# Optimization experiments

Hardware: AMD Instinct MI355X
Metric: run time of the kernel (lower is better)

Reference implementation:

```python
import jax, jax.numpy as jnp
import numpy as np

B, N, D = 64, 2048, 128  # batch, neighbors, embedding_dim (= region_dim)


def setup_inputs() -> dict:
    key = jax.random.key(0)
    ks = jax.random.split(key, 8)
    inv_sqrt_d = 1.0 / np.sqrt(D).astype(np.float32)
    return {
        "e_i": jax.random.normal(ks[0], (B, D), jnp.float32),
        "e_j": jax.random.normal(ks[1], (B, N, D), jnp.float32),
        "imp_j": jax.random.uniform(ks[2], (B, N), jnp.float32),
        "R_lk": jax.random.normal(ks[3], (D, D), jnp.float32),
        "W_q": jax.random.normal(ks[4], (D, D), jnp.float32) * inv_sqrt_d,
        "W_k": jax.random.normal(ks[5], (D, D), jnp.float32) * inv_sqrt_d,
        "W_v": jax.random.normal(ks[6], (D, D), jnp.float32) * inv_sqrt_d,
        "omega": jax.random.normal(ks[7], (D,), jnp.float32),
    }


def reference(e_i, e_j, imp_j, R_lk, W_q, W_k, W_v, omega):
    # torch nn.Linear(x) = x @ W.T; weights are [out, in] = [D, D]
    q = e_i @ W_q.T                                   # [B, D]
    k = jnp.einsum('bnd,ed->bne', e_j, W_k)           # [B, N, D]
    # additive tanh attention score sigma_ij = tanh(q_i + k_j) . omega
    sigma = jnp.tanh(q[:, None, :] + k) @ omega       # [B, N]
    exp_s = jnp.exp(sigma)
    denom = jnp.sum(exp_s, axis=1, keepdims=True) + 1e-9
    a = imp_j * exp_s / denom                         # [B, N]  (a_ij, squeezed)
    v = jnp.einsum('bnd,ed->bne', e_j, W_v)           # [B, N, D]
    # A_i_t = sum_n a_ij * v_j  (identical math to A_i_l in the source)
    A_l = jnp.einsum('bn,bnd->bd', a, v)              # [B, D]
    # sum_n R[l,k] * a[b,n] * v[b,n,k] = R[l,k] * A_l[b,k]  -- fused, no [B,N,D,D]
    A_lk = R_lk[None, :, :] * A_l[:, None, :]         # [B, D, D]
    return A_l, A_lk, A_l
```

## Files before the change

kernel.cpp:

```cpp
#include <hip/hip_runtime.h>
#include <stdint.h>

#define BB 64
#define NN 2048
#define DD 128
#define ROWS 64
#define CPB 2

typedef __attribute__((ext_vector_type(8))) short short8;
typedef __attribute__((ext_vector_type(4))) float f32x4;

__device__ __forceinline__ unsigned short f2bf_rtne(float x) {
    union { float f; unsigned int u; } v; v.f = x;
    unsigned int r = v.u + 0x7fffu + ((v.u >> 16) & 1u);
    return (unsigned short)(r >> 16);
}
__device__ __forceinline__ float bf2f(unsigned short h) {
    union { unsigned int u; float f; } v; v.u = ((unsigned int)h) << 16;
    return v.f;
}
__device__ __forceinline__ float tanh_fast(float x) {
    float ax = fabsf(x);
    float e  = __expf(-2.f * ax);
    float t  = (1.f - e) / (1.f + e);
    return copysignf(t, x);
}
__device__ __forceinline__ void ldsbar() {
    asm volatile("s_waitcnt lgkmcnt(0)" ::: "memory");
    __builtin_amdgcn_s_barrier();
}

__global__ __launch_bounds__(256) void aegis_prep(
    const float* __restrict__ e_i, const float* __restrict__ Wq,
    const float* __restrict__ Wk,
    float* __restrict__ qbuf, unsigned short* __restrict__ Bhig,
    unsigned short* __restrict__ Blog,
    float* __restrict__ sprime, float* __restrict__ denom)
{
    __shared__ float eis[DD];
    const int t = threadIdx.x, blk = blockIdx.x;
    if (blk < 8) {
        const int tid = blk * 256 + t;
        const int lr = tid & 15, lg = (tid >> 4) & 3, ks = (tid >> 6) & 3, et = tid >> 8;
        const int e = et * 16 + lr, k = ks * 32 + lg * 8;
        const float* src = Wk + e * DD + k;
        float4 x0 = *reinterpret_cast<const float4*>(src);
        float4 x1 = *reinterpret_cast<const float4*>(src + 4);
        float xs[8] = {x0.x, x0.y, x0.z, x0.w, x1.x, x1.y, x1.z, x1.w};
        short8 h, l;
        #pragma unroll
        for (int j = 0; j < 8; ++j) {
            unsigned short hb = f2bf_rtne(xs[j]);
            float rem = xs[j] - bf2f(hb);
            h[j] = (short)hb;
            l[j] = (short)f2bf_rtne(rem);
        }
        *reinterpret_cast<short8*>(Bhig + (size_t)tid * 8) = h;
        *reinterpret_cast<short8*>(Blog + (size_t)tid * 8) = l;
    } else {
        const int b = blk - 8;
        if (t < DD) eis[t] = e_i[b * DD + t];
        __syncthreads();
        if (t < DD) {
            float acc = 0.f;
            const float4* wr = reinterpret_cast<const float4*>(Wq + t * DD);
            const float4* ev = reinterpret_cast<const float4*>(eis);
            #pragma unroll 8
            for (int i = 0; i < 32; ++i) {
                float4 w = wr[i], e = ev[i];
                acc = fmaf(w.x, e.x, acc); acc = fmaf(w.y, e.y, acc);
                acc = fmaf(w.z, e.z, acc); acc = fmaf(w.w, e.w, acc);
            }
            qbuf[b * DD + t] = acc;
            sprime[b * DD + t] = 0.f;
        }
        if (t == 0) denom[b] = 0.f;
    }
}

__global__ __launch_bounds__(256, 3) void aegis_main(
    const float* __restrict__ e_j, const float* __restrict__ imp,
    const float* __restrict__ omega, const float* __restrict__ qbuf,
    const unsigned short* __restrict__ Bhig, const unsigned short* __restrict__ Blog,
    float* __restrict__ sprime, float* __restrict__ denom)
{
    __shared__ unsigned short Ehi[ROWS * DD];
    __shared__ unsigned short Elo[ROWS * DD];
    __shared__ float sig[ROWS][4];
    __shared__ float wrow[ROWS];
    __shared__ float scolq[4][DD];

    const int t    = threadIdx.x;
    const int b    = blockIdx.x >> 4;
    const int cb   = blockIdx.x & 15;
    const int lane = t & 63;
    const int w    = t >> 6;
    const int lr   = lane & 15;
    const int lg   = lane >> 4;
    const int row0 = cb * (CPB * ROWS);

    float4 st[8];
    const float4* ejp = reinterpret_cast<const float4*>(
        e_j + (size_t)(b * NN + row0) * DD);
    #pragma unroll
    for (int i = 0; i < 8; ++i) st[i] = ejp[t + i * 256];

    short8 Bh[2][4], Bl[2][4];
    #pragma unroll
    for (int ct = 0; ct < 2; ++ct)
        #pragma unroll
        for (int ks = 0; ks < 4; ++ks) {
            const int fi = (((2 * w + ct) * 4 + ks) * 4 + lg) * 16 + lr;
            Bh[ct][ks] = *reinterpret_cast<const short8*>(Bhig + (size_t)fi * 8);
            Bl[ct][ks] = *reinterpret_cast<const short8*>(Blog + (size_t)fi * 8);
        }

    float qv[2], ov[2];
    #pragma unroll
    for (int ct = 0; ct < 2; ++ct) {
        const int c = 32 * w + 16 * ct + lr;
        qv[ct] = qbuf[b * DD + c];
        ov[ct] = omega[c];
    }
    float impv[CPB];
    if (t < ROWS) {
        #pragma unroll
        for (int c = 0; c < CPB; ++c) impv[c] = imp[b * NN + row0 + c * ROWS + t];
    }

    #pragma unroll
    for (int i = 0; i < 8; ++i) {
        const int idx = t + i * 256;
        const int rr  = idx >> 5;
        const int bc  = (idx & 31) * 8;
        float xs[4] = {st[i].x, st[i].y, st[i].z, st[i].w};
        unsigned short hs[4], ls[4];
        #pragma unroll
        for (int j = 0; j < 4; ++j) {
            hs[j] = f2bf_rtne(xs[j]);
            ls[j] = f2bf_rtne(xs[j] - bf2f(hs[j]));
        }
        uint2 ph, pl;
        ph.x = (unsigned)hs[0] | ((unsigned)hs[1] << 16);
        ph.y = (unsigned)hs[2] | ((unsigned)hs[3] << 16);
        pl.x = (unsigned)ls[0] | ((unsigned)ls[1] << 16);
        pl.y = (unsigned)ls[2] | ((unsigned)ls[3] << 16);
        const int off = rr * 256 + (bc ^ ((rr & 7) << 4));
        *reinterpret_cast<uint2*>(reinterpret_cast<char*>(Ehi) + off) = ph;
        *reinterpret_cast<uint2*>(reinterpret_cast<char*>(Elo) + off) = pl;
    }
    #pragma unroll
    for (int i = 0; i < 8; ++i) st[i] = ejp[2048 + t + i * 256];

    ldsbar();

    float sacc = 0.f, den_local = 0.f;
    const int rq = t >> 6;
    const int cp = t & 63;

    #pragma unroll
    for (int c = 0; c < CPB; ++c) {
        #pragma unroll 1
        for (int rt = 0; rt < 4; ++rt) {
            f32x4 a0 = {0.f, 0.f, 0.f, 0.f};
            f32x4 a1 = {0.f, 0.f, 0.f, 0.f};
            const int arow  = rt * 16 + lr;
            const int rbase = arow * 256;
            const int rsw   = (lr & 7) << 4;
            #pragma unroll
            for (int ks = 0; ks < 4; ++ks) {
                const int off = rbase + ((ks * 64 + lg * 16) ^ rsw);
                short8 ah = *reinterpret_cast<const short8*>(
                    reinterpret_cast<const char*>(Ehi) + off);
                short8 al = *reinterpret_cast<const short8*>(
                    reinterpret_cast<const char*>(Elo) + off);
                a0 = __builtin_amdgcn_mfma_f32_16x16x32_bf16(ah, Bh[0][ks], a0, 0, 0, 0);
                a1 = __builtin_amdgcn_mfma_f32_16x16x32_bf16(ah, Bh[1][ks], a1, 0, 0, 0);
                a0 = __builtin_amdgcn_mfma_f32_16x16x32_bf16(ah, Bl[0][ks], a0, 0, 0, 0);
                a1 = __builtin_amdgcn_mfma_f32_16x16x32_bf16(ah, Bl[1][ks], a1, 0, 0, 0);
                a0 = __builtin_amdgcn_mfma_f32_16x16x32_bf16(al, Bh[0][ks], a0, 0, 0, 0);
                a1 = __builtin_amdgcn_mfma_f32_16x16x32_bf16(al, Bh[1][ks], a1, 0, 0, 0);
            }
            float sp[4];
            #pragma unroll
            for (int i = 0; i < 4; ++i) {
                float x0 = qv[0] + a0[i];
                float x1 = qv[1] + a1[i];
                sp[i] = fmaf(ov[0], tanh_fast(x0), ov[1] * tanh_fast(x1));
            }
            #pragma unroll
            for (int m = 1; m < 16; m <<= 1) {
                #pragma unroll
                for (int i = 0; i < 4; ++i) sp[i] += __shfl_xor(sp[i], m);
            }
            if (lr == 0) {
                #pragma unroll
                for (int i = 0; i < 4; ++i) sig[rt * 16 + 4 * lg + i][w] = sp[i];
            }
        }
        ldsbar();

        if (t < ROWS) {
            float sg = sig[t][0] + sig[t][1] + sig[t][2] + sig[t][3];
            float es = __expf(sg);
            wrow[t]  = es * impv[c];
            float ds = es;
            #pragma unroll
            for (int m = 1; m < 64; m <<= 1) ds += __shfl_xor(ds, m);
            if (t == 0) den_local += ds;
        }
        ldsbar();

        {
            float a0 = 0.f, a1 = 0.f;
            #pragma unroll
            for (int j = 0; j < 16; ++j) {
                const int rr  = rq * 16 + j;
                const int off = rr * 256 + ((4 * cp) ^ ((rr & 7) << 4));
                const unsigned hbits = *reinterpret_cast<const unsigned*>(
                    reinterpret_cast<const char*>(Ehi) + off);
                const unsigned lbits = *reinterpret_cast<const unsigned*>(
                    reinterpret_cast<const char*>(Elo) + off);
                const float wv = wrow[rr];
                float v0 = bf2f((unsigned short)hbits) + bf2f((unsigned short)lbits);
                float v1 = bf2f((unsigned short)(hbits >> 16)) + bf2f((unsigned short)(lbits >> 16));
                a0 = fmaf(wv, v0, a0);
                a1 = fmaf(wv, v1, a1);
            }
            scolq[rq][2 * cp]     = a0;
            scolq[rq][2 * cp + 1] = a1;
        }
        ldsbar();

        if (t < DD) sacc += scolq[0][t] + scolq[1][t] + scolq[2][t] + scolq[3][t];

        if (c + 1 < CPB) {
            #pragma unroll
            for (int i = 0; i < 8; ++i) {
                const int idx = t + i * 256;
                const int rr  = idx >> 5;
                const int bc  = (idx & 31) * 8;
                float xs[4] = {st[i].x, st[i].y, st[i].z, st[i].w};
                unsigned short hs[4], ls[4];
                #pragma unroll
                for (int j = 0; j < 4; ++j) {
                    hs[j] = f2bf_rtne(xs[j]);
                    ls[j] = f2bf_rtne(xs[j] - bf2f(hs[j]));
                }
                uint2 ph, pl;
                ph.x = (unsigned)hs[0] | ((unsigned)hs[1] << 16);
                ph.y = (unsigned)hs[2] | ((unsigned)hs[3] << 16);
                pl.x = (unsigned)ls[0] | ((unsigned)ls[1] << 16);
                pl.y = (unsigned)ls[2] | ((unsigned)ls[3] << 16);
                const int off = rr * 256 + (bc ^ ((rr & 7) << 4));
                *reinterpret_cast<uint2*>(reinterpret_cast<char*>(Ehi) + off) = ph;
                *reinterpret_cast<uint2*>(reinterpret_cast<char*>(Elo) + off) = pl;
            }
            ldsbar();
        }
    }

    if (t < DD) atomicAdd(&sprime[b * DD + t], sacc);
    if (t == 0) atomicAdd(&denom[b], den_local);
}

__global__ __launch_bounds__(256) void aegis_epi(
    const float* __restrict__ sprime, const float* __restrict__ denomv,
    const float* __restrict__ Wv, const float* __restrict__ R,
    float* __restrict__ out)
{
    __shared__ float sn[DD];
    __shared__ float alred[DD][2];
    __shared__ float al[DD];
    const int t = threadIdx.x, b = blockIdx.x;

    if (t < DD) sn[t] = sprime[b * DD + t] / (denomv[b] + 1e-9f);
    __syncthreads();
    {
        const int l = t >> 1, h = t & 1;
        const float4* wr = reinterpret_cast<const float4*>(Wv + l * DD + h * 64);
        const float4* sv = reinterpret_cast<const float4*>(sn + h * 64);
        float acc = 0.f;
        #pragma unroll 8
        for (int i = 0; i < 16; ++i) {
            float4 w = wr[i], e = sv[i];
            acc = fmaf(w.x, e.x, acc); acc = fmaf(w.y, e.y, acc);
            acc = fmaf(w.z, e.z, acc); acc = fmaf(w.w, e.w, acc);
        }
        alred[l][h] = acc;
    }
    __syncthreads();
    if (t < DD) {
        float v = alred[t][0] + alred[t][1];
        al[t] = v;
        out[b * DD + t] = v;
        out[8192 + 1048576 + b * DD + t] = v;
    }
    __syncthreads();
    float4* dst = reinterpret_cast<float4*>(out + 8192 + (size_t)b * DD * DD);
    const float4* rsrc = reinterpret_cast<const float4*>(R);
    #pragma unroll
    for (int i = 0; i < 16; ++i) {
        const int idx = t + i * 256;
        float4 r = rsrc[idx];
        const int k0 = (idx & 31) * 4;
        float4 o;
        o.x = r.x * al[k0];     o.y = r.y * al[k0 + 1];
        o.z = r.z * al[k0 + 2]; o.w = r.w * al[k0 + 3];
        dst[idx] = o;
    }
}

extern "C" void kernel_launch(void* const* d_in, const int* in_sizes, int n_in,
                              void* d_out, int out_size, void* d_ws, size_t ws_size,
                              hipStream_t stream) {
    const float* e_i = (const float*)d_in[0];
    const float* e_j = (const float*)d_in[1];
    const float* imp = (const float*)d_in[2];
    const float* R   = (const float*)d_in[3];
    const float* Wq  = (const float*)d_in[4];
    const float* Wk  = (const float*)d_in[5];
    const float* Wv  = (const float*)d_in[6];
    const float* om  = (const float*)d_in[7];

    float* out    = (float*)d_out;
    float* sprime = (float*)d_ws;
    float* denom  = (float*)((char*)d_ws + 32768);

    float* qbuf = out + 8192;
    unsigned short* Bhig = (unsigned short*)(out + 8192 + 8192);
    unsigned short* Blog = Bhig + 16384;

    aegis_prep<<<dim3(72), dim3(256), 0, stream>>>(
        e_i, Wq, Wk, qbuf, Bhig, Blog, sprime, denom);
    aegis_main<<<dim3(BB * 16), dim3(256), 0, stream>>>(
        e_j, imp, om, qbuf, Bhig, Blog, sprime, denom);
    aegis_epi<<<dim3(BB), dim3(256), 0, stream>>>(sprime, denom, Wv, R, out);
}
```

Baseline: 153.3 us.

## Process one 64-row chunk per block and double the main-kernel grid

The main kernel now gives each block a single 64-row chunk instead of two, and launches twice as many blocks (BB*32). This removes the in-block register prefetch of the second chunk and the per-chunk loop, so each block needs fewer registers, and the launch bound no longer requests three blocks per CU. The cost is twice as many atomicAdds into sprime and denom, plus the setup repeated in every block (loading the B fragments, q and omega). The block also loses its overlap of the next chunk's global load with the current chunk's compute.

Measured after the change: 133.9 us. 1.15x faster.

```diff
diff --git a/kernel.cpp b/kernel.cpp
--- a/kernel.cpp
+++ b/kernel.cpp
@@ -5,7 +5,6 @@
 #define NN 2048
 #define DD 128
 #define ROWS 64
-#define CPB 2
 
 typedef __attribute__((ext_vector_type(8))) short short8;
 typedef __attribute__((ext_vector_type(4))) float f32x4;
@@ -78,7 +77,7 @@
     }
 }
 
-__global__ __launch_bounds__(256, 3) void aegis_main(
+__global__ __launch_bounds__(256) void aegis_main(
     const float* __restrict__ e_j, const float* __restrict__ imp,
     const float* __restrict__ omega, const float* __restrict__ qbuf,
     const unsigned short* __restrict__ Bhig, const unsigned short* __restrict__ Blog,
@@ -90,14 +89,14 @@
     __shared__ float wrow[ROWS];
     __shared__ float scolq[4][DD];
 
-    const int t    = threadIdx.x;
-    const int b    = blockIdx.x >> 4;
-    const int cb   = blockIdx.x & 15;
-    const int lane = t & 63;
-    const int w    = t >> 6;
-    const int lr   = lane & 15;
-    const int lg   = lane >> 4;
-    const int row0 = cb * (CPB * ROWS);
+    const int t     = threadIdx.x;
+    const int b     = blockIdx.x >> 5;
+    const int chunk = blockIdx.x & 31;
+    const int row0  = chunk * ROWS;
+    const int lane  = t & 63;
+    const int w     = t >> 6;
+    const int lr    = lane & 15;
+    const int lg    = lane >> 4;
 
     float4 st[8];
     const float4* ejp = reinterpret_cast<const float4*>(
@@ -122,11 +121,7 @@
         qv[ct] = qbuf[b * DD + c];
         ov[ct] = omega[c];
     }
-    float impv[CPB];
-    if (t < ROWS) {
-        #pragma unroll
-        for (int c = 0; c < CPB; ++c) impv[c] = imp[b * NN + row0 + c * ROWS + t];
-    }
+    const float impv = (t < ROWS) ? imp[b * NN + row0 + t] : 0.f;
 
     #pragma unroll
     for (int i = 0; i < 8; ++i) {
@@ -149,118 +144,86 @@
         *reinterpret_cast<uint2*>(reinterpret_cast<char*>(Ehi) + off) = ph;
         *reinterpret_cast<uint2*>(reinterpret_cast<char*>(Elo) + off) = pl;
     }
-    #pragma unroll
-    for (int i = 0; i < 8; ++i) st[i] = ejp[2048 + t + i * 256];
-
     ldsbar();
 
-    float sacc = 0.f, den_local = 0.f;
-    const int rq = t >> 6;
-    const int cp = t & 63;
-
-    #pragma unroll
-    for (int c = 0; c < CPB; ++c) {
-        #pragma unroll 1
-        for (int rt = 0; rt < 4; ++rt) {
-            f32x4 a0 = {0.f, 0.f, 0.f, 0.f};
-            f32x4 a1 = {0.f, 0.f, 0.f, 0.f};
-            const int arow  = rt * 16 + lr;
-            const int rbase = arow * 256;
-            const int rsw   = (lr & 7) << 4;
+    #pragma unroll 1
+    for (int rt = 0; rt < 4; ++rt) {
+        f32x4 a0 = {0.f, 0.f, 0.f, 0.f};
+        f32x4 a1 = {0.f, 0.f, 0.f, 0.f};
+        const int rbase = (rt * 16 + lr) * 256;
+        const int rsw   = (lr & 7) << 4;
+        #pragma unroll
+        for (int ks = 0; ks < 4; ++ks) {
+            const int off = rbase + ((ks * 64 + lg * 16) ^ rsw);
+            short8 ah = *reinterpret_cast<const short8*>(
+                reinterpret_cast<const char*>(Ehi) + off);
+            short8 al = *reinterpret_cast<const short8*>(
+                reinterpret_cast<const char*>(Elo) + off);
+            a0 = __builtin_amdgcn_mfma_f32_16x16x32_bf16(ah, Bh[0][ks], a0, 0, 0, 0);
+            a1 = __builtin_amdgcn_mfma_f32_16x16x32_bf16(ah, Bh[1][ks], a1, 0, 0, 0);
+            a0 = __builtin_amdgcn_mfma_f32_16x16x32_bf16(ah, Bl[0][ks], a0, 0, 0, 0);
+            a1 = __builtin_amdgcn_mfma_f32_16x16x32_bf16(ah, Bl[1][ks], a1, 0, 0, 0);
+            a0 = __builtin_amdgcn_mfma_f32_16x16x32_bf16(al, Bh[0][ks], a0, 0, 0, 0);
+            a1 = __builtin_amdgcn_mfma_f32_16x16x32_bf16(al, Bh[1][ks], a1, 0, 0, 0);
+        }
+        float sp[4];
+        #pragma unroll
+        for (int i = 0; i < 4; ++i) {
+            float x0 = qv[0] + a0[i];
+            float x1 = qv[1] + a1[i];
+            sp[i] = fmaf(ov[0], tanh_fast(x0), ov[1] * tanh_fast(x1));
+        }
+        #pragma unroll
+        for (int m = 1; m < 16; m <<= 1) {
             #pragma unroll
-            for (int ks = 0; ks < 4; ++ks) {
-                const int off = rbase + ((ks * 64 + lg * 16) ^ rsw);
-                short8 ah = *reinterpret_cast<const short8*>(
-                    reinterpret_cast<const char*>(Ehi) + off);
-                short8 al = *reinterpret_cast<const short8*>(
-                    reinterpret_cast<const char*>(Elo) + off);
-                a0 = __builtin_amdgcn_mfma_f32_16x16x32_bf16(ah, Bh[0][ks], a0, 0, 0, 0);
-                a1 = __builtin_amdgcn_mfma_f32_16x16x32_bf16(ah, Bh[1][ks], a1, 0, 0, 0);
-                a0 = __builtin_amdgcn_mfma_f32_16x16x32_bf16(ah, Bl[0][ks], a0, 0, 0, 0);
-                a1 = __builtin_amdgcn_mfma_f32_16x16x32_bf16(ah, Bl[1][ks], a1, 0, 0, 0);
-                a0 = __builtin_amdgcn_mfma_f32_16x16x32_bf16(al, Bh[0][ks], a0, 0, 0, 0);
-                a1 = __builtin_amdgcn_mfma_f32_16x16x32_bf16(al, Bh[1][ks], a1, 0, 0, 0);
-            }
-            float sp[4];
+            for (int i = 0; i < 4; ++i) sp[i] += __shfl_xor(sp[i], m);
+        }
+        if (lr == 0) {
             #pragma unroll
-            for (int i = 0; i < 4; ++i) {
-                float x0 = qv[0] + a0[i];
-                float x1 = qv[1] + a1[i];
-                sp[i] = fmaf(ov[0], tanh_fast(x0), ov[1] * tanh_fast(x1));
-            }
-            #pragma unroll
-            for (int m = 1; m < 16; m <<= 1) {
-                #pragma unroll
-                for (int i = 0; i < 4; ++i) sp[i] += __shfl_xor(sp[i], m);
-            }
-            if (lr == 0) {
-                #pragma unroll
-                for (int i = 0; i < 4; ++i) sig[rt * 16 + 4 * lg + i][w] = sp[i];
-            }
-        }
-        ldsbar();
-
-        if (t < ROWS) {
-            float sg = sig[t][0] + sig[t][1] + sig[t][2] + sig[t][3];
-            float es = __expf(sg);
-            wrow[t]  = es * impv[c];
-            float ds = es;
-            #pragma unroll
-            for (int m = 1; m < 64; m <<= 1) ds += __shfl_xor(ds, m);
-            if (t == 0) den_local += ds;
-        }
-        ldsbar();
-
-        {
-            float a0 = 0.f, a1 = 0.f;
-            #pragma unroll
-            for (int j = 0; j < 16; ++j) {
-                const int rr  = rq * 16 + j;
-                const int off = rr * 256 + ((4 * cp) ^ ((rr & 7) << 4));
-                const unsigned hbits = *reinterpret_cast<const unsigned*>(
-                    reinterpret_cast<const char*>(Ehi) + off);
-                const unsigned lbits = *reinterpret_cast<const unsigned*>(
-                    reinterpret_cast<const char*>(Elo) + off);
-                const float wv = wrow[rr];
-                float v0 = bf2f((unsigned short)hbits) + bf2f((unsigned short)lbits);
-                float v1 = bf2f((unsigned short)(hbits >> 16)) + bf2f((unsigned short)(lbits >> 16));
-                a0 = fmaf(wv, v0, a0);
-                a1 = fmaf(wv, v1, a1);
-            }
-            scolq[rq][2 * cp]     = a0;
-            scolq[rq][2 * cp + 1] = a1;
-        }
-        ldsbar();
-
-        if (t < DD) sacc += scolq[0][t] + scolq[1][t] + scolq[2][t] + scolq[3][t];
-
-        if (c + 1 < CPB) {
-            #pragma unroll
-            for (int i = 0; i < 8; ++i) {
-                const int idx = t + i * 256;
-                const int rr  = idx >> 5;
-                const int bc  = (idx & 31) * 8;
-                float xs[4] = {st[i].x, st[i].y, st[i].z, st[i].w};
-                unsigned short hs[4], ls[4];
-                #pragma unroll
-                for (int j = 0; j < 4; ++j) {
-                    hs[j] = f2bf_rtne(xs[j]);
-                    ls[j] = f2bf_rtne(xs[j] - bf2f(hs[j]));
-                }
-                uint2 ph, pl;
-                ph.x = (unsigned)hs[0] | ((unsigned)hs[1] << 16);
-                ph.y = (unsigned)hs[2] | ((unsigned)hs[3] << 16);
-                pl.x = (unsigned)ls[0] | ((unsigned)ls[1] << 16);
-                pl.y = (unsigned)ls[2] | ((unsigned)ls[3] << 16);
-                const int off = rr * 256 + (bc ^ ((rr & 7) << 4));
-                *reinterpret_cast<uint2*>(reinterpret_cast<char*>(Ehi) + off) = ph;
-                *reinterpret_cast<uint2*>(reinterpret_cast<char*>(Elo) + off) = pl;
-            }
-            ldsbar();
-        }
-    }
-
-    if (t < DD) atomicAdd(&sprime[b * DD + t], sacc);
+            for (int i = 0; i < 4; ++i) sig[rt * 16 + 4 * lg + i][w] = sp[i];
+        }
+    }
+    ldsbar();
+
+    float den_local = 0.f;
+    if (t < ROWS) {
+        float sg = sig[t][0] + sig[t][1] + sig[t][2] + sig[t][3];
+        float es = __expf(sg);
+        wrow[t]  = es * impv;
+        float ds = es;
+        #pragma unroll
+        for (int m = 1; m < 64; m <<= 1) ds += __shfl_xor(ds, m);
+        den_local = ds;
+    }
+    ldsbar();
+
+    {
+        const int rq = t >> 6;
+        const int cp = t & 63;
+        float a0 = 0.f, a1 = 0.f;
+        #pragma unroll
+        for (int j = 0; j < 16; ++j) {
+            const int rr  = rq * 16 + j;
+            const int off = rr * 256 + ((4 * cp) ^ ((rr & 7) << 4));
+            const unsigned hbits = *reinterpret_cast<const unsigned*>(
+                reinterpret_cast<const char*>(Ehi) + off);
+            const unsigned lbits = *reinterpret_cast<const unsigned*>(
+                reinterpret_cast<const char*>(Elo) + off);
+            const float wv = wrow[rr];
+            float v0 = bf2f((unsigned short)hbits) + bf2f((unsigned short)lbits);
+            float v1 = bf2f((unsigned short)(hbits >> 16)) + bf2f((unsigned short)(lbits >> 16));
+            a0 = fmaf(wv, v0, a0);
+            a1 = fmaf(wv, v1, a1);
+        }
+        scolq[rq][2 * cp]     = a0;
+        scolq[rq][2 * cp + 1] = a1;
+    }
+    ldsbar();
+
+    if (t < DD) {
+        const float s = scolq[0][t] + scolq[1][t] + scolq[2][t] + scolq[3][t];
+        atomicAdd(&sprime[b * DD + t], s);
+    }
     if (t == 0) atomicAdd(&denom[b], den_local);
 }
 
@@ -333,7 +296,7 @@
 
     aegis_prep<<<dim3(72), dim3(256), 0, stream>>>(
         e_i, Wq, Wk, qbuf, Bhig, Blog, sprime, denom);
-    aegis_main<<<dim3(BB * 16), dim3(256), 0, stream>>>(
+    aegis_main<<<dim3(BB * 32), dim3(256), 0, stream>>>(
         e_j, imp, om, qbuf, Bhig, Blog, sprime, denom);
     aegis_epi<<<dim3(BB), dim3(256), 0, stream>>>(sprime, denom, Wv, R, out);
 }
```
